# Kernel optimization log

Hardware: AMD Instinct MI355X
Metric: run time of the kernel (lower is better)

The kernel has to match this reference:

```python
import jax, jax.numpy as jnp
import numpy as np

B, C, D, H, W = 2, 512, 32, 32, 32
L, CTX = 256, 768
NH, HD, G = 8, 64, 8
EPS = 1e-5


def group_norm(x, w, b):
    Bb, Cc, Dd, Hh, Ww = x.shape
    xg = x.reshape(Bb, G, Cc // G, Dd, Hh, Ww)
    mu = xg.mean(axis=(2, 3, 4, 5), keepdims=True)
    var = xg.var(axis=(2, 3, 4, 5), keepdims=True)
    xn = ((xg - mu) * jax.lax.rsqrt(var + EPS)).reshape(Bb, Cc, Dd, Hh, Ww)
    return xn * w[None, :, None, None, None] + b[None, :, None, None, None]


def layer_norm(x, w, b):
    mu = x.mean(axis=-1, keepdims=True)
    var = x.var(axis=-1, keepdims=True)
    return (x - mu) * jax.lax.rsqrt(var + EPS) * w + b


def setup_inputs() -> dict:
    key = jax.random.key(0)
    ks = jax.random.split(key, 8)
    s = 0.02  # weight init scale
    return {
        "x": jax.random.normal(ks[0], (B, C, D, H, W), jnp.float32),
        "context": jax.random.normal(ks[1], (B, L, CTX), jnp.float32),
        "gn_w": jnp.ones((C,), jnp.float32),
        "gn_b": jnp.zeros((C,), jnp.float32),
        "ln_w": jnp.ones((CTX,), jnp.float32),
        "ln_b": jnp.zeros((CTX,), jnp.float32),
        "q_w": jax.random.normal(ks[2], (C, C), jnp.float32) * s,
        "q_b": jnp.zeros((C,), jnp.float32),
        "k_w": jax.random.normal(ks[3], (C, CTX), jnp.float32) * s,
        "k_b": jnp.zeros((C,), jnp.float32),
        "v_w": jax.random.normal(ks[4], (C, CTX), jnp.float32) * s,
        "v_b": jnp.zeros((C,), jnp.float32),
        "proj_w": jax.random.normal(ks[5], (C, C), jnp.float32) * s,
        "proj_b": jnp.zeros((C,), jnp.float32),
    }


def reference(x, context, gn_w, gn_b, ln_w, ln_b, q_w, q_b, k_w, k_b, v_w, v_b, proj_w, proj_b):
    Bb, Cc, Dd, Hh, Ww = x.shape
    S = Dd * Hh * Ww
    h = group_norm(x, gn_w, gn_b)
    ctx = layer_norm(context, ln_w, ln_b)
    # 1x1 Conv3d == per-voxel linear over channels
    q = jnp.einsum('oc,bcdhw->bodhw', q_w, h) + q_b[None, :, None, None, None]
    q = q.reshape(Bb, NH, HD, S)                                        # (b,h,e,s)
    k = (ctx @ k_w.T + k_b).reshape(Bb, L, NH, HD).transpose(0, 2, 1, 3)  # (b,h,l,e)
    v = (ctx @ v_w.T + v_b).reshape(Bb, L, NH, HD).transpose(0, 2, 1, 3)  # (b,h,l,e)
    scale = HD ** -0.5
    attn = jnp.einsum('bhes,bhle->bhsl', q, k) * scale                  # (b,h,S,L)
    attn = jax.nn.softmax(attn, axis=-1)
    out = jnp.einsum('bhsl,bhle->bhes', attn, v).reshape(Bb, Cc, Dd, Hh, Ww)
    out = jnp.einsum('oc,bcdhw->bodhw', proj_w, out) + proj_b[None, :, None, None, None]
    return out + x
```

## Files before the change

kernel.cpp:

```cpp
#include <hip/hip_runtime.h>

typedef unsigned short u16;
typedef unsigned int u32;
typedef __attribute__((ext_vector_type(4))) float f32x4;
typedef __attribute__((ext_vector_type(8))) short bf16x8;
typedef __attribute__((ext_vector_type(8))) u16 u16x8;
typedef __attribute__((ext_vector_type(4))) u16 u16x4;
typedef __attribute__((ext_vector_type(4))) u32 u32x4;

#define DEVI __device__ __forceinline__

constexpr int C_ = 512, S_ = 32768, L_ = 256, CTX_ = 768;

DEVI u16 f2b(float f) {
    union { float f; unsigned u; } x; x.f = f;
    unsigned r = x.u + 0x7fffu + ((x.u >> 16) & 1u);
    return (u16)(r >> 16);
}

DEVI f32x4 mfma16(bf16x8 a, bf16x8 b, f32x4 c) {
    return __builtin_amdgcn_mfma_f32_16x16x32_bf16(a, b, c, 0, 0, 0);
}

DEVI void gload16(const void* g, void* l) {
    __builtin_amdgcn_global_load_lds(
        (const __attribute__((address_space(1))) void*)g,
        (__attribute__((address_space(3))) void*)l, 16, 0, 0);
}

DEVI u32 cvtpk(float lo, float hi) {
    u32 d;
    asm("v_cvt_pk_bf16_f32 %0, %1, %2" : "=v"(d) : "v"(lo), "v"(hi));
    return d;
}
DEVI void pl32(u32& a, u32& b) {
    asm volatile("v_permlane32_swap_b32 %0, %1" : "+v"(a), "+v"(b));
}
DEVI void pl16(u32& a, u32& b) {
    asm volatile("v_permlane16_swap_b32 %0, %1" : "+v"(a), "+v"(b));
}

__global__ __launch_bounds__(256) void cvt_w(
    const float* __restrict__ a0, const float* __restrict__ a1,
    const float* __restrict__ a2, const float* __restrict__ a3,
    u16* __restrict__ o0, u16* __restrict__ o1,
    u16* __restrict__ o2, u16* __restrict__ o3)
{
    int which = blockIdx.y;
    const float* src = which == 0 ? a0 : which == 1 ? a1 : which == 2 ? a2 : a3;
    u16* dst = which == 0 ? o0 : which == 1 ? o1 : which == 2 ? o2 : o3;
    int n4 = (which == 1 || which == 2) ? (512 * 768 / 4) : (512 * 512 / 4);
    int i = blockIdx.x * 256 + threadIdx.x;
    if (i < n4) {
        float4 v = ((const float4*)src)[i];
        u16x4 o; o[0] = f2b(v.x); o[1] = f2b(v.y); o[2] = f2b(v.z); o[3] = f2b(v.w);
        ((u16x4*)dst)[i] = o;
    }
}

__global__ __launch_bounds__(256) void gn_partial(const float* __restrict__ x,
                                                  float* __restrict__ part)
{
    const int bg = blockIdx.y, blk = blockIdx.x, tid = threadIdx.x;
    const float* base = x + (size_t)bg * 64 * S_ + (size_t)blk * 1024 + tid * 4;
    float s1 = 0.f, s2 = 0.f;
    for (int c = 0; c < 64; ++c) {
        float4 v = *(const float4*)(base + (size_t)c * S_);
        s1 += v.x + v.y + v.z + v.w;
        s2 += v.x * v.x + v.y * v.y + v.z * v.z + v.w * v.w;
    }
    for (int m = 1; m < 64; m <<= 1) { s1 += __shfl_xor(s1, m); s2 += __shfl_xor(s2, m); }
    __shared__ float a1[4], a2[4];
    int w = tid >> 6, lane = tid & 63;
    if (lane == 0) { a1[w] = s1; a2[w] = s2; }
    __syncthreads();
    if (tid == 0) {
        part[(bg * 32 + blk) * 2 + 0] = a1[0] + a1[1] + a1[2] + a1[3];
        part[(bg * 32 + blk) * 2 + 1] = a2[0] + a2[1] + a2[2] + a2[3];
    }
}

__global__ __launch_bounds__(64) void gn_final(const float* __restrict__ part,
                                               float* __restrict__ stats)
{
    int bg = blockIdx.x, tid = threadIdx.x;
    float s1 = tid < 32 ? part[(bg * 32 + tid) * 2] : 0.f;
    float s2 = tid < 32 ? part[(bg * 32 + tid) * 2 + 1] : 0.f;
    for (int m = 1; m < 32; m <<= 1) { s1 += __shfl_xor(s1, m); s2 += __shfl_xor(s2, m); }
    if (tid == 0) {
        const float invN = 1.0f / (64.0f * (float)S_);
        float mu = s1 * invN, var = s2 * invN - mu * mu;
        stats[bg * 2] = mu;
        stats[bg * 2 + 1] = rsqrtf(var + 1e-5f);
    }
}

__global__ __launch_bounds__(256) void gn_apply(
    const float* __restrict__ x, const float* __restrict__ stats,
    const float* __restrict__ gw, const float* __restrict__ gb,
    u16* __restrict__ ht)
{
    __shared__ float tile[64][65];
    const int tid = threadIdx.x, sl = tid & 63, c4 = tid >> 6;
    const int s0 = blockIdx.x * 64, c0 = blockIdx.y * 64, b = blockIdx.z;
    const int bg = b * 8 + (c0 >> 6);
    const float mu = stats[bg * 2], rstd = stats[bg * 2 + 1];
#pragma unroll
    for (int i = 0; i < 16; ++i) {
        int cl = c4 * 16 + i;
        float wv = gw[c0 + cl], bv = gb[c0 + cl];
        float v = x[((size_t)(b * C_ + c0 + cl)) * S_ + s0 + sl];
        tile[sl][cl] = (v - mu) * rstd * wv + bv;
    }
    __syncthreads();
#pragma unroll
    for (int i = 0; i < 16; ++i) {
        int so = c4 * 16 + i;
        ht[((size_t)(b * S_ + s0 + so)) * C_ + c0 + sl] = f2b(tile[so][sl]);
    }
}

__global__ __launch_bounds__(256) void ln_ctx(
    const float* __restrict__ ctx, const float* __restrict__ lw,
    const float* __restrict__ lb, u16* __restrict__ cn)
{
    const int row = blockIdx.x, tid = threadIdx.x;
    const float* p = ctx + (size_t)row * CTX_;
    float v0 = p[tid], v1 = p[tid + 256], v2 = p[tid + 512];
    float s1 = v0 + v1 + v2, s2 = v0 * v0 + v1 * v1 + v2 * v2;
    for (int m = 1; m < 64; m <<= 1) { s1 += __shfl_xor(s1, m); s2 += __shfl_xor(s2, m); }
    __shared__ float a1[4], a2[4];
    int w = tid >> 6, lane = tid & 63;
    if (lane == 0) { a1[w] = s1; a2[w] = s2; }
    __syncthreads();
    s1 = a1[0] + a1[1] + a1[2] + a1[3];
    s2 = a2[0] + a2[1] + a2[2] + a2[3];
    const float invN = 1.0f / 768.0f;
    float mu = s1 * invN, rstd = rsqrtf(s2 * invN - mu * mu + 1e-5f);
    u16* o = cn + (size_t)row * CTX_;
    o[tid]       = f2b((v0 - mu) * rstd * lw[tid]       + lb[tid]);
    o[tid + 256] = f2b((v1 - mu) * rstd * lw[tid + 256] + lb[tid + 256]);
    o[tid + 512] = f2b((v2 - mu) * rstd * lw[tid + 512] + lb[tid + 512]);
}

template <int MODE, bool SWAP>
__global__ __launch_bounds__(256, 4) void gemm_nt(
    const u16* __restrict__ A, const u16* __restrict__ Bp,
    const float* __restrict__ bias, void* __restrict__ outp,
    const float* __restrict__ resid, int K, int ldo,
    size_t aStride, size_t bStride, size_t oStride, float scale,
    const u16* __restrict__ Bp2, const float* __restrict__ bias2,
    void* __restrict__ outp2)
{
    __shared__ __align__(16) u16 lA[2][4096];
    __shared__ __align__(16) u16 lB[2][4096];
    const int tid = threadIdx.x;
    const int w = tid >> 6, lane = tid & 63;
    const int g = lane >> 4, r = lane & 15;

    const int nx = gridDim.x, nxy = nx * gridDim.y;
    const int raw = blockIdx.x + nx * blockIdx.y;
    const int tile = (raw & 7) * (nxy >> 3) + (raw >> 3);
    const int bx = tile % nx, by = tile / nx;
    const int m0 = (SWAP ? by : bx) * 128, n0 = (SWAP ? bx : by) * 128;
    const int z = blockIdx.z;
    A += (size_t)z * aStride;
    const u16* Bsel = Bp;
    if constexpr (MODE == 3) { if (z) Bsel = Bp2; }
    Bsel += (size_t)z * bStride;

    const int l8 = lane & 7, lh = lane >> 3;
    const int u_ = l8 ^ lh;
    const int mro = (lh << 1) + (u_ >> 2);
    const int kco = (u_ & 3) * 8;
    const int wr = w >> 1, wc = w & 1;
    const int nt = K >> 5;

    f32x4 acc[4][4];
#pragma unroll
    for (int m = 0; m < 4; ++m)
#pragma unroll
        for (int n = 0; n < 4; ++n) acc[m][n] = f32x4{0.f, 0.f, 0.f, 0.f};

#define STAGE_T(t, bi_) {                                                      \
    size_t ko_ = (size_t)((t) * 32 + kco);                                     \
    _Pragma("unroll")                                                          \
    for (int j = 0; j < 2; ++j) {                                              \
        int grow_ = w * 32 + j * 16 + mro;                                     \
        gload16(A + (size_t)(m0 + grow_) * K + ko_,                            \
                &lA[bi_][(w * 16 + j * 8) << 6]);                              \
        gload16(Bsel + (size_t)(n0 + grow_) * K + ko_,                         \
                &lB[bi_][(w * 16 + j * 8) << 6]);                              \
    } }

    STAGE_T(0, 0);
    __syncthreads();

    for (int t = 0; t < nt; ++t) {
        const int cur = t & 1;
        if (t + 1 < nt) STAGE_T(t + 1, cur ^ 1);
        bf16x8 af[4], bf_[4];
#pragma unroll
        for (int m = 0; m < 4; ++m) {
            int row = wr * 32 + m * 8 + (r >> 1);
            int slot = (((r & 1) << 2) + g) ^ ((r >> 1) & 7);
            af[m] = *(const bf16x8*)&lA[cur][(row << 6) + (slot << 3)];
        }
#pragma unroll
        for (int n = 0; n < 4; ++n) {
            int row = wc * 32 + n * 8 + (r >> 1);
            int slot = (((r & 1) << 2) + g) ^ ((r >> 1) & 7);
            bf_[n] = *(const bf16x8*)&lB[cur][(row << 6) + (slot << 3)];
        }
#pragma unroll
        for (int m = 0; m < 4; ++m)
#pragma unroll
            for (int n = 0; n < 4; ++n)
                acc[m][n] = mfma16(af[m], bf_[n], acc[m][n]);
        __syncthreads();
    }
#undef STAGE_T

    if constexpr (MODE == 0) {
        u16* ob = (u16*)outp + (size_t)z * oStride;
#pragma unroll
        for (int n = 0; n < 4; ++n) {
            int gn = n0 + wc * 64 + n * 16 + r;
            float bn = bias[gn] * scale;
#pragma unroll
            for (int m = 0; m < 4; ++m) {
                int gm = m0 + wr * 64 + m * 16 + g * 4;
#pragma unroll
                for (int i = 0; i < 4; ++i)
                    ob[(size_t)(gm + i) * ldo + gn] = f2b(acc[m][n][i] * scale + bn);
            }
        }
    } else if constexpr (MODE == 2) {
        float* of = (float*)outp + (size_t)z * oStride;
        const float* rs = resid + (size_t)z * oStride;
#pragma unroll
        for (int m = 0; m < 4; ++m) {
            int gm = m0 + wr * 64 + m * 16 + g * 4;
#pragma unroll
            for (int i = 0; i < 4; ++i) {
                float bm = bias[gm + i];
#pragma unroll
                for (int n = 0; n < 4; ++n) {
                    int gn = n0 + wc * 64 + n * 16 + r;
                    size_t idx = (size_t)(gm + i) * ldo + gn;
                    of[idx] = acc[m][n][i] + bm + rs[idx];
                }
            }
        }
    } else if constexpr (MODE == 3) {
        if (z == 0) {
            u16* ob = (u16*)outp;
#pragma unroll
            for (int n = 0; n < 4; ++n) {
                int gn = n0 + wc * 64 + n * 16 + r;
                float bn = bias[gn];
#pragma unroll
                for (int m = 0; m < 4; ++m) {
                    int gm = m0 + wr * 64 + m * 16 + g * 4;
#pragma unroll
                    for (int i = 0; i < 4; ++i)
                        ob[(size_t)(gm + i) * ldo + gn] = f2b(acc[m][n][i] + bn);
                }
            }
        } else {
            u16* ob = (u16*)outp2;
#pragma unroll
            for (int n = 0; n < 4; ++n) {
                int gn = n0 + wc * 64 + n * 16 + r;
                float bn = bias2[gn];
#pragma unroll
                for (int m = 0; m < 4; ++m) {
                    int gm = m0 + wr * 64 + m * 16 + g * 4;
                    int bb = gm >> 8, l = gm & 255;
                    u16x4 pk;
#pragma unroll
                    for (int i = 0; i < 4; ++i) pk[i] = f2b(acc[m][n][i] + bn);
                    *(u16x4*)&ob[((size_t)(bb * 512 + gn)) * 256 + l] = pk;
                }
            }
        }
    }
}

__global__ __launch_bounds__(256, 2) void attn_kernel(
    const u16* __restrict__ q, const u16* __restrict__ kk,
    const u16* __restrict__ vv, u16* __restrict__ ao)
{
    __shared__ __align__(16) u16 sm[32768];
    const int tid = threadIdx.x;
    const int w = tid >> 6, lane = tid & 63;
    const int g = lane >> 4, r = lane & 15;
    const int bh = blockIdx.y, b = bh >> 3, h = bh & 7;
    const int s0 = blockIdx.x * 128;

    {
        const u16* kbase = kk + ((size_t)b * L_) * C_ + h * 64;
#pragma unroll
        for (int j = 0; j < 8; ++j) {
            int idx = j * 256 + tid;
            int l = idx >> 3, ch = idx & 7;
            u16x8 val = *(const u16x8*)(kbase + (size_t)l * C_ + ch * 8);
            *(u16x8*)&sm[l * 64 + ((ch ^ (l & 7)) << 3)] = val;
        }
        const u16* vbase = vv + ((size_t)bh * 64) * 256;
#pragma unroll
        for (int j = 0; j < 8; ++j) {
            int idx = j * 256 + tid;
            int e = idx >> 5, ch = idx & 31;
            u16x8 val = *(const u16x8*)(vbase + (size_t)e * 256 + ch * 8);
            *(u16x8*)&sm[16384 + e * 256 + ((ch ^ (e & 7)) << 3)] = val;
        }
    }

    const int sw = s0 + w * 32;
    bf16x8 qf[2][2];
#pragma unroll
    for (int m = 0; m < 2; ++m)
#pragma unroll
        for (int kt = 0; kt < 2; ++kt)
            qf[m][kt] = *(const bf16x8*)(q + ((size_t)(b * S_ + sw + m * 16 + r)) * C_
                                         + h * 64 + kt * 32 + g * 8);
    __syncthreads();

    f32x4 accs[2][16];
#pragma unroll
    for (int m = 0; m < 2; ++m)
#pragma unroll
        for (int n = 0; n < 16; ++n) accs[m][n] = f32x4{0.f, 0.f, 0.f, 0.f};
    __builtin_amdgcn_s_setprio(1);
#pragma unroll
    for (int n = 0; n < 16; ++n) {
#pragma unroll
        for (int kt = 0; kt < 2; ++kt) {
            int c = kt * 4 + g;
            bf16x8 kf = *(const bf16x8*)&sm[(n * 16 + r) * 64 + ((c ^ (r & 7)) << 3)];
#pragma unroll
            for (int m = 0; m < 2; ++m) accs[m][n] = mfma16(kf, qf[m][kt], accs[m][n]);
        }
    }
    __builtin_amdgcn_s_setprio(0);

    float inv[2];
#pragma unroll
    for (int m = 0; m < 2; ++m) {
        float mx = accs[m][0][0];
#pragma unroll
        for (int n = 0; n < 16; ++n)
#pragma unroll
            for (int i = 0; i < 4; ++i) mx = fmaxf(mx, accs[m][n][i]);
        mx = fmaxf(mx, __shfl_xor(mx, 16));
        mx = fmaxf(mx, __shfl_xor(mx, 32));
        float sum = 0.f;
#pragma unroll
        for (int n = 0; n < 16; ++n)
#pragma unroll
            for (int i = 0; i < 4; ++i) {
                float e = __expf(accs[m][n][i] - mx);
                accs[m][n][i] = e; sum += e;
            }
        sum += __shfl_xor(sum, 16);
        sum += __shfl_xor(sum, 32);
        inv[m] = 1.0f / sum;
    }

    f32x4 acco[2][4];
#pragma unroll
    for (int m = 0; m < 2; ++m)
#pragma unroll
        for (int n = 0; n < 4; ++n) acco[m][n] = f32x4{0.f, 0.f, 0.f, 0.f};

#pragma unroll
    for (int c = 0; c < 8; ++c) {
        bf16x8 pa[2];
#pragma unroll
        for (int m = 0; m < 2; ++m) {
            u32 x0 = cvtpk(accs[m][2 * c][0] * inv[m], accs[m][2 * c][1] * inv[m]);
            u32 x1 = cvtpk(accs[m][2 * c][2] * inv[m], accs[m][2 * c][3] * inv[m]);
            u32 y0 = cvtpk(accs[m][2 * c + 1][0] * inv[m], accs[m][2 * c + 1][1] * inv[m]);
            u32 y1 = cvtpk(accs[m][2 * c + 1][2] * inv[m], accs[m][2 * c + 1][3] * inv[m]);
            pl32(x0, y0);
            pl32(x1, y1);
            pl16(x0, y0);
            pl16(x1, y1);
            u32x4 pw; pw[0] = x0; pw[1] = x1; pw[2] = y0; pw[3] = y1;
            pa[m] = *(bf16x8*)&pw;
        }
        bf16x8 vf[4];
#pragma unroll
        for (int n = 0; n < 4; ++n) {
            int e = n * 16 + r;
            vf[n] = *(const bf16x8*)&sm[16384 + e * 256 + (((c * 4 + g) ^ (r & 7)) << 3)];
        }
        __builtin_amdgcn_s_setprio(1);
#pragma unroll
        for (int m = 0; m < 2; ++m)
#pragma unroll
            for (int n = 0; n < 4; ++n)
                acco[m][n] = mfma16(pa[m], vf[n], acco[m][n]);
        __builtin_amdgcn_s_setprio(0);
    }

#pragma unroll
    for (int m = 0; m < 2; ++m)
#pragma unroll
        for (int n = 0; n < 4; ++n)
#pragma unroll
            for (int i = 0; i < 4; ++i) {
                int s = sw + m * 16 + g * 4 + i;
                int e = n * 16 + r;
                ao[((size_t)(b * S_ + s)) * C_ + h * 64 + e] = f2b(acco[m][n][i]);
            }
}

extern "C" void kernel_launch(void* const* d_in, const int* in_sizes, int n_in,
                              void* d_out, int out_size, void* d_ws, size_t ws_size,
                              hipStream_t stream)
{
    (void)in_sizes; (void)n_in; (void)out_size; (void)ws_size;
    const float* x    = (const float*)d_in[0];
    const float* ctx  = (const float*)d_in[1];
    const float* gn_w = (const float*)d_in[2];
    const float* gn_b = (const float*)d_in[3];
    const float* ln_w = (const float*)d_in[4];
    const float* ln_b = (const float*)d_in[5];
    const float* q_w  = (const float*)d_in[6];
    const float* q_b  = (const float*)d_in[7];
    const float* k_w  = (const float*)d_in[8];
    const float* k_b  = (const float*)d_in[9];
    const float* v_w  = (const float*)d_in[10];
    const float* v_b  = (const float*)d_in[11];
    const float* p_w  = (const float*)d_in[12];
    const float* p_b  = (const float*)d_in[13];
    float* out = (float*)d_out;

    char* ws = (char*)d_ws;
    constexpr size_t WS_WQ   = 0;
    constexpr size_t WS_WK   = WS_WQ + (size_t)512 * 512 * 2;
    constexpr size_t WS_WV   = WS_WK + (size_t)512 * 768 * 2;
    constexpr size_t WS_WP   = WS_WV + (size_t)512 * 768 * 2;
    constexpr size_t WS_PART = WS_WP + (size_t)512 * 512 * 2;
    constexpr size_t WS_STAT = WS_PART + (size_t)16 * 64 * 2 * 4;
    constexpr size_t WS_CTXN = WS_STAT + 256;
    constexpr size_t WS_K    = WS_CTXN + (size_t)512 * 768 * 2;
    constexpr size_t WS_V    = WS_K + (size_t)2 * 8 * 256 * 64 * 2;
    constexpr size_t WS_Q    = WS_V + (size_t)2 * 8 * 256 * 64 * 2;
    constexpr size_t WS_H    = WS_Q + (size_t)2 * 32768 * 512 * 2;

    u16* wq = (u16*)(ws + WS_WQ);
    u16* wk = (u16*)(ws + WS_WK);
    u16* wv = (u16*)(ws + WS_WV);
    u16* wp = (u16*)(ws + WS_WP);
    float* part  = (float*)(ws + WS_PART);
    float* stats = (float*)(ws + WS_STAT);
    u16* ctxn = (u16*)(ws + WS_CTXN);
    u16* kt   = (u16*)(ws + WS_K);
    u16* vt   = (u16*)(ws + WS_V);
    u16* qt   = (u16*)(ws + WS_Q);
    u16* ht   = (u16*)(ws + WS_H);
    u16* ao   = ht;

    const size_t bsc = (size_t)S_ * C_;

    cvt_w<<<dim3(384, 4), 256, 0, stream>>>(q_w, k_w, v_w, p_w, wq, wk, wv, wp);
    gn_partial<<<dim3(32, 16), 256, 0, stream>>>(x, part);
    gn_final<<<16, 64, 0, stream>>>(part, stats);
    gn_apply<<<dim3(512, 8, 2), 256, 0, stream>>>(x, stats, gn_w, gn_b, ht);
    ln_ctx<<<512, 256, 0, stream>>>(ctx, ln_w, ln_b, ctxn);
    gemm_nt<0, true><<<dim3(4, 256, 2), 256, 0, stream>>>(
        ht, wq, q_b, qt, nullptr, 512, 512, bsc, 0, bsc, 0.125f,
        nullptr, nullptr, nullptr);
    gemm_nt<3, false><<<dim3(4, 4, 2), 256, 0, stream>>>(
        ctxn, wk, k_b, kt, nullptr, 768, 512, 0, 0, 0, 1.0f,
        wv, v_b, vt);
    attn_kernel<<<dim3(256, 16), 256, 0, stream>>>(qt, kt, vt, ao);
    gemm_nt<2, false><<<dim3(4, 256, 2), 256, 0, stream>>>(
        wp, ao, p_b, out, x, 512, S_, 0, bsc, bsc, 1.0f,
        nullptr, nullptr, nullptr);
}
```

Baseline: 279.5 us.

## Vectorize epilogue stores via swapped MFMA operands and read V from global

Swaps the A/B operands of the MFMA calls in the GEMM and in attention so that each lane holds four contiguous output columns. The epilogues can then write packed 8-byte bf16 or 16-byte float4 stores instead of scalar strided stores. The group-norm transpose kernel now writes 16-byte vectors. Attention no longer stages V in LDS: it reads V fragments straight from global/L2, which halves shared memory and raises the occupancy hint to 4 blocks per SM, at the cost of repeated uncoalesced global reads of V.

```diff
diff --git a/kernel.cpp b/kernel.cpp
--- a/kernel.cpp
+++ b/kernel.cpp
@@ -114,9 +114,13 @@
     }
     __syncthreads();
 #pragma unroll
-    for (int i = 0; i < 16; ++i) {
-        int so = c4 * 16 + i;
-        ht[((size_t)(b * S_ + s0 + so)) * C_ + c0 + sl] = f2b(tile[so][sl]);
+    for (int rep = 0; rep < 2; ++rep) {
+        int task = rep * 256 + tid;
+        int so = task >> 3, cb = task & 7;
+        u16x8 o;
+#pragma unroll
+        for (int j = 0; j < 8; ++j) o[j] = f2b(tile[so][cb * 8 + j]);
+        *(u16x8*)&ht[((size_t)(b * S_ + s0 + so)) * C_ + c0 + cb * 8] = o;
     }
 }
 
@@ -216,7 +220,7 @@
         for (int m = 0; m < 4; ++m)
 #pragma unroll
             for (int n = 0; n < 4; ++n)
-                acc[m][n] = mfma16(af[m], bf_[n], acc[m][n]);
+                acc[m][n] = mfma16(bf_[n], af[m], acc[m][n]);
         __syncthreads();
     }
 #undef STAGE_T
@@ -224,15 +228,17 @@
     if constexpr (MODE == 0) {
         u16* ob = (u16*)outp + (size_t)z * oStride;
 #pragma unroll
-        for (int n = 0; n < 4; ++n) {
-            int gn = n0 + wc * 64 + n * 16 + r;
-            float bn = bias[gn] * scale;
-#pragma unroll
-            for (int m = 0; m < 4; ++m) {
-                int gm = m0 + wr * 64 + m * 16 + g * 4;
-#pragma unroll
-                for (int i = 0; i < 4; ++i)
-                    ob[(size_t)(gm + i) * ldo + gn] = f2b(acc[m][n][i] * scale + bn);
+        for (int m = 0; m < 4; ++m) {
+            int gm = m0 + wr * 64 + m * 16 + r;
+#pragma unroll
+            for (int n = 0; n < 4; ++n) {
+                int gn0 = n0 + wc * 64 + n * 16 + g * 4;
+                float4 bn = *(const float4*)&bias[gn0];
+                u32 w0 = cvtpk(acc[m][n][0] * scale + bn.x * scale,
+                               acc[m][n][1] * scale + bn.y * scale);
+                u32 w1 = cvtpk(acc[m][n][2] * scale + bn.z * scale,
+                               acc[m][n][3] * scale + bn.w * scale);
+                *(uint2*)&ob[(size_t)gm * ldo + gn0] = make_uint2(w0, w1);
             }
         }
     } else if constexpr (MODE == 2) {
@@ -240,58 +246,60 @@
         const float* rs = resid + (size_t)z * oStride;
 #pragma unroll
         for (int m = 0; m < 4; ++m) {
-            int gm = m0 + wr * 64 + m * 16 + g * 4;
-#pragma unroll
-            for (int i = 0; i < 4; ++i) {
-                float bm = bias[gm + i];
-#pragma unroll
-                for (int n = 0; n < 4; ++n) {
-                    int gn = n0 + wc * 64 + n * 16 + r;
-                    size_t idx = (size_t)(gm + i) * ldo + gn;
-                    of[idx] = acc[m][n][i] + bm + rs[idx];
-                }
+            int gm = m0 + wr * 64 + m * 16 + r;
+            float bm = bias[gm];
+#pragma unroll
+            for (int n = 0; n < 4; ++n) {
+                int gn0 = n0 + wc * 64 + n * 16 + g * 4;
+                size_t idx = (size_t)gm * ldo + gn0;
+                float4 rv = *(const float4*)&rs[idx];
+                float4 o4;
+                o4.x = acc[m][n][0] + bm + rv.x;
+                o4.y = acc[m][n][1] + bm + rv.y;
+                o4.z = acc[m][n][2] + bm + rv.z;
+                o4.w = acc[m][n][3] + bm + rv.w;
+                *(float4*)&of[idx] = o4;
             }
         }
     } else if constexpr (MODE == 3) {
         if (z == 0) {
             u16* ob = (u16*)outp;
 #pragma unroll
-            for (int n = 0; n < 4; ++n) {
-                int gn = n0 + wc * 64 + n * 16 + r;
-                float bn = bias[gn];
-#pragma unroll
-                for (int m = 0; m < 4; ++m) {
-                    int gm = m0 + wr * 64 + m * 16 + g * 4;
-#pragma unroll
-                    for (int i = 0; i < 4; ++i)
-                        ob[(size_t)(gm + i) * ldo + gn] = f2b(acc[m][n][i] + bn);
+            for (int m = 0; m < 4; ++m) {
+                int gm = m0 + wr * 64 + m * 16 + r;
+#pragma unroll
+                for (int n = 0; n < 4; ++n) {
+                    int gn0 = n0 + wc * 64 + n * 16 + g * 4;
+                    float4 bn = *(const float4*)&bias[gn0];
+                    u32 w0 = cvtpk(acc[m][n][0] + bn.x, acc[m][n][1] + bn.y);
+                    u32 w1 = cvtpk(acc[m][n][2] + bn.z, acc[m][n][3] + bn.w);
+                    *(uint2*)&ob[(size_t)gm * ldo + gn0] = make_uint2(w0, w1);
                 }
             }
         } else {
             u16* ob = (u16*)outp2;
 #pragma unroll
-            for (int n = 0; n < 4; ++n) {
-                int gn = n0 + wc * 64 + n * 16 + r;
-                float bn = bias2[gn];
-#pragma unroll
-                for (int m = 0; m < 4; ++m) {
-                    int gm = m0 + wr * 64 + m * 16 + g * 4;
-                    int bb = gm >> 8, l = gm & 255;
-                    u16x4 pk;
-#pragma unroll
-                    for (int i = 0; i < 4; ++i) pk[i] = f2b(acc[m][n][i] + bn);
-                    *(u16x4*)&ob[((size_t)(bb * 512 + gn)) * 256 + l] = pk;
+            for (int m = 0; m < 4; ++m) {
+                int gm = m0 + wr * 64 + m * 16 + r;
+                int bb = gm >> 8, l = gm & 255;
+#pragma unroll
+                for (int n = 0; n < 4; ++n) {
+                    int gn0 = n0 + wc * 64 + n * 16 + g * 4;
+#pragma unroll
+                    for (int i = 0; i < 4; ++i)
+                        ob[((size_t)(bb * 512 + gn0 + i)) * 256 + l] =
+                            f2b(acc[m][n][i] + bias2[gn0 + i]);
                 }
             }
         }
     }
 }
 
-__global__ __launch_bounds__(256, 2) void attn_kernel(
+__global__ __launch_bounds__(256, 4) void attn_kernel(
     const u16* __restrict__ q, const u16* __restrict__ kk,
     const u16* __restrict__ vv, u16* __restrict__ ao)
 {
-    __shared__ __align__(16) u16 sm[32768];
+    __shared__ __align__(16) u16 sm[16384];
     const int tid = threadIdx.x;
     const int w = tid >> 6, lane = tid & 63;
     const int g = lane >> 4, r = lane & 15;
@@ -306,14 +314,6 @@
             int l = idx >> 3, ch = idx & 7;
             u16x8 val = *(const u16x8*)(kbase + (size_t)l * C_ + ch * 8);
             *(u16x8*)&sm[l * 64 + ((ch ^ (l & 7)) << 3)] = val;
-        }
-        const u16* vbase = vv + ((size_t)bh * 64) * 256;
-#pragma unroll
-        for (int j = 0; j < 8; ++j) {
-            int idx = j * 256 + tid;
-            int e = idx >> 5, ch = idx & 31;
-            u16x8 val = *(const u16x8*)(vbase + (size_t)e * 256 + ch * 8);
-            *(u16x8*)&sm[16384 + e * 256 + ((ch ^ (e & 7)) << 3)] = val;
         }
     }
 
@@ -374,6 +374,7 @@
 #pragma unroll
         for (int n = 0; n < 4; ++n) acco[m][n] = f32x4{0.f, 0.f, 0.f, 0.f};
 
+    const u16* vbase = vv + ((size_t)bh * 64) * 256;
 #pragma unroll
     for (int c = 0; c < 8; ++c) {
         bf16x8 pa[2];
@@ -392,29 +393,27 @@
         }
         bf16x8 vf[4];
 #pragma unroll
+        for (int n = 0; n < 4; ++n)
+            vf[n] = *(const bf16x8*)(vbase + ((size_t)(n * 16 + r)) * 256 + (c * 4 + g) * 8);
+        __builtin_amdgcn_s_setprio(1);
+#pragma unroll
+        for (int m = 0; m < 2; ++m)
+#pragma unroll
+            for (int n = 0; n < 4; ++n)
+                acco[m][n] = mfma16(vf[n], pa[m], acco[m][n]);
+        __builtin_amdgcn_s_setprio(0);
+    }
+
+#pragma unroll
+    for (int m = 0; m < 2; ++m) {
+        const size_t rowb = ((size_t)(b * S_ + sw + m * 16 + r)) * C_ + h * 64;
+#pragma unroll
         for (int n = 0; n < 4; ++n) {
-            int e = n * 16 + r;
-            vf[n] = *(const bf16x8*)&sm[16384 + e * 256 + (((c * 4 + g) ^ (r & 7)) << 3)];
-        }
-        __builtin_amdgcn_s_setprio(1);
-#pragma unroll
-        for (int m = 0; m < 2; ++m)
-#pragma unroll
-            for (int n = 0; n < 4; ++n)
-                acco[m][n] = mfma16(pa[m], vf[n], acco[m][n]);
-        __builtin_amdgcn_s_setprio(0);
-    }
-
-#pragma unroll
-    for (int m = 0; m < 2; ++m)
-#pragma unroll
-        for (int n = 0; n < 4; ++n)
-#pragma unroll
-            for (int i = 0; i < 4; ++i) {
-                int s = sw + m * 16 + g * 4 + i;
-                int e = n * 16 + r;
-                ao[((size_t)(b * S_ + s)) * C_ + h * 64 + e] = f2b(acco[m][n][i]);
-            }
+            u32 w0 = cvtpk(acco[m][n][0], acco[m][n][1]);
+            u32 w1 = cvtpk(acco[m][n][2], acco[m][n][3]);
+            *(uint2*)&ao[rowb + n * 16 + g * 4] = make_uint2(w0, w1);
+        }
+    }
 }
 
 extern "C" void kernel_launch(void* const* d_in, const int* in_sizes, int n_in,
```

Result: slower. 463.0 us (+65.6%).
